# Optimization experiments

Hardware: AMD Instinct MI355X
Metric: run time of the kernel (lower is better)

## Reference

```python
import math
import jax, jax.numpy as jnp
import numpy as np

NUM_HEAD = 16
BLOCK_SIZE = 2048

def get_slopes(n):
    def pow2(n):
        start = 2 ** (-2 ** (-(math.log2(n) - 3)))
        return [start * start ** i for i in range(n)]
    if math.log2(n).is_integer():
        return pow2(n)
    c = 2 ** math.floor(math.log2(n))
    return pow2(c) + get_slopes(2 * c)[0::2][: n - c]

def setup_inputs() -> dict:
    key = jax.random.key(0)
    ks = jax.random.split(key, 5)
    B, T, C = 4, 2048, 1024
    x = jax.random.normal(ks[0], (B, T, C), dtype=jnp.float32)
    Wq = 0.02 * jax.random.normal(ks[1], (C, C), dtype=jnp.float32)
    Wk = 0.02 * jax.random.normal(ks[2], (C, C), dtype=jnp.float32)
    Wv = 0.02 * jax.random.normal(ks[3], (C, C), dtype=jnp.float32)
    Wo = 0.02 * jax.random.normal(ks[4], (C, C), dtype=jnp.float32)
    return {"x": x, "Wq": Wq, "Wk": Wk, "Wv": Wv, "Wo": Wo}

def reference(x, Wq, Wk, Wv, Wo):
    B, T, C = x.shape
    nh, hd = NUM_HEAD, C // NUM_HEAD
    # projections, split heads -> [B, nh, T, hd]
    q = (x @ Wq).reshape(B, T, nh, hd).transpose(0, 2, 1, 3)
    k = (x @ Wk).reshape(B, T, nh, hd).transpose(0, 2, 1, 3)
    v = (x @ Wv).reshape(B, T, nh, hd).transpose(0, 2, 1, 3)
    # full [B, nh, T, T] scores (module materializes these)
    attn = jnp.einsum("bhqd,bhkd->bhqk", q, k) / jnp.sqrt(jnp.float32(hd))
    # ALiBi bias as in create_mask: slope * (j - (block_size - 1)), key-position only
    slopes = jnp.asarray(get_slopes(nh), dtype=jnp.float32)  # [nh]
    bias = slopes[:, None] * (jnp.arange(T, dtype=jnp.float32) - (BLOCK_SIZE - 1))  # [nh, T]
    attn = attn + bias[None, :, None, :]
    # causal mask + stable softmax in fp32
    causal = jnp.tril(jnp.ones((T, T), dtype=bool))
    masked = jnp.where(causal[None, None], attn.astype(jnp.float32), jnp.finfo(jnp.float32).min)
    probs = jax.nn.softmax(masked, axis=-1)
    out = jnp.einsum("bhqk,bhkd->bhqd", probs, v)  # [B, nh, T, hd]
    out = out.transpose(0, 2, 1, 3).reshape(B, T, C)
    return out @ Wo
```

## Files before the change

### kernel.cpp

```cpp
#include <hip/hip_runtime.h>
#include <hip/hip_bf16.h>

#define TSEQ   2048
#define CDIM   1024
#define NHEAD  16
#define HDIM   64

typedef float f32x4  __attribute__((ext_vector_type(4)));
typedef float f32x16v __attribute__((ext_vector_type(16)));
typedef __bf16 bf16x8 __attribute__((ext_vector_type(8)));
typedef unsigned short u16x8 __attribute__((ext_vector_type(8)));
typedef unsigned short u16x4 __attribute__((ext_vector_type(4)));
typedef unsigned int   u32x4 __attribute__((ext_vector_type(4)));

#define QSCALE 0.18033688011112042f
#define LOG2E  1.4426950408889634f

static __device__ __forceinline__ unsigned short f2bf(float f) {
    unsigned u = __builtin_bit_cast(unsigned, f);
    unsigned r = u + 0x7FFFu + ((u >> 16) & 1u);
    return (unsigned short)(r >> 16);
}

static __device__ __forceinline__ f32x4 mfma16(u16x8 a, u16x8 b, f32x4 c) {
    return __builtin_amdgcn_mfma_f32_16x16x32_bf16(
        __builtin_bit_cast(bf16x8, a), __builtin_bit_cast(bf16x8, b), c, 0, 0, 0);
}
static __device__ __forceinline__ f32x16v mfma32(u16x8 a, u16x8 b, f32x16v c) {
    return __builtin_amdgcn_mfma_f32_32x32x16_bf16(
        __builtin_bit_cast(bf16x8, a), __builtin_bit_cast(bf16x8, b), c, 0, 0, 0);
}

static __device__ __forceinline__ void gload16(const void* g, void* l) {
    __builtin_amdgcn_global_load_lds(
        (const __attribute__((address_space(1))) unsigned int*)g,
        (__attribute__((address_space(3))) unsigned int*)l, 16, 0, 0);
}


__global__ __launch_bounds__(256) void castx(
    const float* __restrict__ x, unsigned short* __restrict__ xb)
{
    int t = blockIdx.x * 256 + threadIdx.x;
    f32x4 v = *(const f32x4*)&x[t * 4];
    u16x4 o;
    o[0] = f2bf(v[0]); o[1] = f2bf(v[1]); o[2] = f2bf(v[2]); o[3] = f2bf(v[3]);
    *(u16x4*)&xb[t * 4] = o;
}

__global__ __launch_bounds__(256) void wtcast(
    const float* __restrict__ wq, const float* __restrict__ wk,
    const float* __restrict__ wv, const float* __restrict__ wo,
    unsigned short* __restrict__ wt)
{
    __shared__ unsigned short t[64 * 72];
    const int z = blockIdx.z;
    const float* src = (z == 0) ? wq : (z == 1) ? wk : (z == 2) ? wv : wo;
    const int k0 = blockIdx.x * 64, n0 = blockIdx.y * 64, tid = threadIdx.x;

    #pragma unroll
    for (int i = 0; i < 4; ++i) {
        int idx = i * 256 + tid;
        int r = idx >> 4, c4 = idx & 15;
        f32x4 v = *(const f32x4*)&src[(k0 + r) * 1024 + n0 + c4 * 4];
        u16x4 o;
        o[0] = f2bf(v[0]); o[1] = f2bf(v[1]); o[2] = f2bf(v[2]); o[3] = f2bf(v[3]);
        *(u16x4*)&t[r * 72 + c4 * 4] = o;
    }
    __syncthreads();
    #pragma unroll
    for (int i = 0; i < 2; ++i) {
        int idx = i * 256 + tid;
        int n = idx >> 3, k8 = idx & 7;
        u16x8 o;
        #pragma unroll
        for (int e = 0; e < 8; ++e) o[e] = t[(k8 * 8 + e) * 72 + n];
        *(u16x8*)&wt[z * 1048576 + (n0 + n) * 1024 + k0 + k8 * 8] = o;
    }
}

template<int MODE>
__global__ __launch_bounds__(256) void gemm_gl(
    const unsigned short* __restrict__ A, const unsigned short* __restrict__ WT,
    unsigned short* __restrict__ outb, float* __restrict__ outf)
{
    __shared__ __align__(16) unsigned short Al[128 * 64];
    __shared__ __align__(16) unsigned short Bl[128 * 64];

    const int tid  = threadIdx.x;
    const int z    = blockIdx.z;
    const int m0   = blockIdx.y * 128;
    const int n0   = blockIdx.x * 128;
    const unsigned short* W = WT + (MODE == 0 ? z * 1048576 : 0);

    const int wid  = tid >> 6, lane = tid & 63;
    const int wr   = (wid >> 1) * 64, wc = (wid & 1) * 64;
    const int lrow = lane & 15, lk = (lane >> 4) * 8;

    f32x4 acc[4][4] = {};

    for (int kt = 0; kt < 16; ++kt) {
        __syncthreads();
        #pragma unroll
        for (int c = 0; c < 4; ++c) {
            int cz = wid * 4 + c;
            int row = cz * 8 + (lane >> 3), col = (lane & 7) * 8;
            gload16(&A[(m0 + row) * 1024 + kt * 64 + col], &Al[cz * 512]);
            gload16(&W[(n0 + row) * 1024 + kt * 64 + col], &Bl[cz * 512]);
        }
        __syncthreads();
        #pragma unroll
        for (int ks = 0; ks < 2; ++ks) {
            u16x8 af[4], bfr[4];
            #pragma unroll
            for (int m = 0; m < 4; ++m)
                af[m] = *(const u16x8*)&Al[(wr + m * 16 + lrow) * 64 + ks * 32 + lk];
            #pragma unroll
            for (int n = 0; n < 4; ++n)
                bfr[n] = *(const u16x8*)&Bl[(wc + n * 16 + lrow) * 64 + ks * 32 + lk];
            #pragma unroll
            for (int m = 0; m < 4; ++m)
                #pragma unroll
                for (int n = 0; n < 4; ++n)
                    acc[m][n] = mfma16(af[m], bfr[n], acc[m][n]);
        }
    }

    const int g = lane >> 4;
    #pragma unroll
    for (int m = 0; m < 4; ++m)
        #pragma unroll
        for (int n = 0; n < 4; ++n)
            #pragma unroll
            for (int j = 0; j < 4; ++j) {
                int grow = m0 + wr + m * 16 + g * 4 + j;
                int gcol = n0 + wc + n * 16 + lrow;
                float val = acc[m][n][j];
                if (MODE == 0) {
                    int b = grow >> 11, t = grow & 2047;
                    int h = gcol >> 6,  d = gcol & 63;
                    if (z == 0) val *= QSCALE;
                    if (z == 2)
                        outb[z * 8388608 + (((b << 4) + h) * 64 + d) * 2048 + t] = f2bf(val);
                    else
                        outb[z * 8388608 + (((b << 4) + h) * 2048 + t) * 64 + d] = f2bf(val);
                } else {
                    outf[grow * 1024 + gcol] = val;
                }
            }
}

__global__ __launch_bounds__(256) void attn32p(
    const unsigned short* __restrict__ qh, const unsigned short* __restrict__ kh,
    const unsigned short* __restrict__ vt, unsigned short* __restrict__ aout)
{
    __shared__ __align__(16) unsigned short Kl[2][64 * 72];
    __shared__ __align__(16) unsigned short Vl[2][64 * 72];

    const int j   = blockIdx.x;
    const int bh  = blockIdx.y;
    const int h   = bh & 15, b = bh >> 4;
    const int tid = threadIdx.x, wid = tid >> 6, lane = tid & 63;
    const int l31 = lane & 31, hi = lane >> 5;

    const int blkA = 15 - j, blkB = j;
    const int ntA  = 2 * blkA + 2;
    const int nt   = 34;

    const unsigned short* Qb = qh + bh * (TSEQ * HDIM);
    const unsigned short* Kb = kh + bh * (TSEQ * HDIM);
    const unsigned short* Vb = vt + bh * (TSEQ * HDIM);

    const float slope2 = exp2f(-0.5f * (float)(h + 1)) * LOG2E;

    int qw = blkA * 128 + wid * 32;
    int qg = qw + l31;
    u16x8 qf[4];
    #pragma unroll
    for (int kf = 0; kf < 4; ++kf)
        qf[kf] = *(const u16x8*)&Qb[qg * 64 + kf * 16 + hi * 8];
    float m_r = -1e30f, l_r = 0.f;
    f32x16v Ot[2] = {};

    #pragma unroll
    for (int i = 0; i < 2; ++i) {
        int idx = i * 256 + tid, row = idx >> 3, c8 = idx & 7;
        *(u16x8*)&Kl[0][row * 72 + c8 * 8] = *(const u16x8*)&Kb[row * 64 + c8 * 8];
        *(u16x8*)&Vl[0][row * 72 + c8 * 8] = *(const u16x8*)&Vb[row * 2048 + c8 * 8];
    }
    int cur = 0;

    for (int t = 0; t < nt; ++t) {
        const int kv0 = (t < ntA ? t : t - ntA) * 64;
        __syncthreads();

        u16x8 kreg[2], vreg[2];
        const bool pre = (t + 1 < nt);
        if (pre) {
            const int t1 = t + 1;
            const int kv0n = (t1 < ntA ? t1 : t1 - ntA) * 64;
            #pragma unroll
            for (int i = 0; i < 2; ++i) {
                int idx = i * 256 + tid, row = idx >> 3, c8 = idx & 7;
                kreg[i] = *(const u16x8*)&Kb[(kv0n + row) * 64 + c8 * 8];
                vreg[i] = *(const u16x8*)&Vb[row * 2048 + kv0n + c8 * 8];
            }
        }

        if (kv0 <= qw + 31) {
            f32x16v st[2];
            __builtin_amdgcn_s_setprio(1);
            #pragma unroll
            for (int kv2 = 0; kv2 < 2; ++kv2) {
                f32x16v a = {};
                #pragma unroll
                for (int kf = 0; kf < 4; ++kf) {
                    u16x8 ka = *(const u16x8*)&Kl[cur][(kv2 * 32 + l31) * 72 + kf * 16 + hi * 8];
                    a = mfma32(ka, qf[kf], a);
                }
                st[kv2] = a;
            }
            __builtin_amdgcn_s_setprio(0);

            const bool diag = (kv0 + 63 > qw);
            #pragma unroll
            for (int kv2 = 0; kv2 < 2; ++kv2) {
                float base = slope2 * (float)(kv0 + kv2 * 32 + 4 * hi - 2047);
                #pragma unroll
                for (int r = 0; r < 16; ++r) {
                    int koff = (r & 3) + 8 * (r >> 2);
                    float v = st[kv2][r] + fmaf(slope2, (float)koff, base);
                    if (diag) {
                        int kv = kv0 + kv2 * 32 + koff + 4 * hi;
                        if (kv > qg) v = -1e30f;
                    }
                    st[kv2][r] = v;
                }
            }

            float t8[8];
            #pragma unroll
            for (int i = 0; i < 8; ++i)
                t8[i] = fmaxf(fmaxf(st[0][i], st[0][i + 8]),
                              fmaxf(st[1][i], st[1][i + 8]));
            #pragma unroll
            for (int i = 0; i < 4; ++i) t8[i] = fmaxf(t8[i], t8[i + 4]);
            float rm = fmaxf(fmaxf(t8[0], t8[1]), fmaxf(t8[2], t8[3]));
            rm = fmaxf(rm, __shfl_xor(rm, 32, 64));

            float mn = fmaxf(m_r, rm);
            float alpha = exp2f(m_r - mn);
            m_r = mn;

            #pragma unroll
            for (int kv2 = 0; kv2 < 2; ++kv2)
                #pragma unroll
                for (int r = 0; r < 16; ++r)
                    st[kv2][r] = exp2f(st[kv2][r] - mn);
            float s8[8];
            #pragma unroll
            for (int i = 0; i < 8; ++i)
                s8[i] = (st[0][i] + st[0][i + 8]) + (st[1][i] + st[1][i + 8]);
            #pragma unroll
            for (int i = 0; i < 4; ++i) s8[i] += s8[i + 4];
            float rs = (s8[0] + s8[1]) + (s8[2] + s8[3]);
            rs += __shfl_xor(rs, 32, 64);
            l_r = l_r * alpha + rs;
            Ot[0] *= alpha;
            Ot[1] *= alpha;

            unsigned pku[2][8];
            #pragma unroll
            for (int kv2 = 0; kv2 < 2; ++kv2)
                #pragma unroll
                for (int idx = 0; idx < 8; ++idx) {
                    unsigned lo = __builtin_bit_cast(unsigned short, (__bf16)st[kv2][2 * idx]);
                    unsigned hh = __builtin_bit_cast(unsigned short, (__bf16)st[kv2][2 * idx + 1]);
                    pku[kv2][idx] = lo | (hh << 16);
                }

            u16x8 pb[4];
            #pragma unroll
            for (int kf = 0; kf < 4; ++kf) {
                const int kv2 = kf >> 1, base = 4 * (kf & 1);
                unsigned s0 = hi ? pku[kv2][base + 0] : pku[kv2][base + 2];
                unsigned s1 = hi ? pku[kv2][base + 1] : pku[kv2][base + 3];
                unsigned r0 = __shfl_xor(s0, 32, 64);
                unsigned r1 = __shfl_xor(s1, 32, 64);
                u32x4 w;
                w[0] = hi ? r0 : pku[kv2][base + 0];
                w[1] = hi ? r1 : pku[kv2][base + 1];
                w[2] = hi ? pku[kv2][base + 2] : r0;
                w[3] = hi ? pku[kv2][base + 3] : r1;
                pb[kf] = __builtin_bit_cast(u16x8, w);
            }

            __builtin_amdgcn_s_setprio(1);
            #pragma unroll
            for (int dn = 0; dn < 2; ++dn) {
                f32x16v o = Ot[dn];
                #pragma unroll
                for (int kf = 0; kf < 4; ++kf) {
                    u16x8 va = *(const u16x8*)&Vl[cur][(dn * 32 + l31) * 72 + kf * 16 + hi * 8];
                    o = mfma32(va, pb[kf], o);
                }
                Ot[dn] = o;
            }
            __builtin_amdgcn_s_setprio(0);
        }

        if (t == ntA - 1) {
            float rl = 1.0f / l_r;
            #pragma unroll
            for (int dn = 0; dn < 2; ++dn)
                #pragma unroll
                for (int rq = 0; rq < 4; ++rq) {
                    u16x4 o;
                    #pragma unroll
                    for (int jj = 0; jj < 4; ++jj)
                        o[jj] = f2bf(Ot[dn][rq * 4 + jj] * rl);
                    int d = dn * 32 + 8 * rq + 4 * hi;
                    *(u16x4*)&aout[(b * 2048 + qg) * 1024 + h * 64 + d] = o;
                }
            qw = blkB * 128 + wid * 32;
            qg = qw + l31;
            #pragma unroll
            for (int kf = 0; kf < 4; ++kf)
                qf[kf] = *(const u16x8*)&Qb[qg * 64 + kf * 16 + hi * 8];
            m_r = -1e30f; l_r = 0.f;
            Ot[0] = (f32x16v){};
            Ot[1] = (f32x16v){};
        }

        if (pre) {
            #pragma unroll
            for (int i = 0; i < 2; ++i) {
                int idx = i * 256 + tid, row = idx >> 3, c8 = idx & 7;
                *(u16x8*)&Kl[cur ^ 1][row * 72 + c8 * 8] = kreg[i];
                *(u16x8*)&Vl[cur ^ 1][row * 72 + c8 * 8] = vreg[i];
            }
        }
        cur ^= 1;
    }

    float rl = 1.0f / l_r;
    #pragma unroll
    for (int dn = 0; dn < 2; ++dn)
        #pragma unroll
        for (int rq = 0; rq < 4; ++rq) {
            u16x4 o;
            #pragma unroll
            for (int jj = 0; jj < 4; ++jj)
                o[jj] = f2bf(Ot[dn][rq * 4 + jj] * rl);
            int d = dn * 32 + 8 * rq + 4 * hi;
            *(u16x4*)&aout[(b * 2048 + qg) * 1024 + h * 64 + d] = o;
        }
}

extern "C" void kernel_launch(void* const* d_in, const int* in_sizes, int n_in,
                              void* d_out, int out_size, void* d_ws, size_t ws_size,
                              hipStream_t stream)
{
    const float* x  = (const float*)d_in[0];
    const float* Wq = (const float*)d_in[1];
    const float* Wk = (const float*)d_in[2];
    const float* Wv = (const float*)d_in[3];
    const float* Wo = (const float*)d_in[4];

    unsigned short* ws = (unsigned short*)d_ws;
    unsigned short* wb = ws;
    unsigned short* xb = ws + 4194304;
    unsigned short* qh = ws + 12582912;
    unsigned short* kh = qh + 8388608;
    unsigned short* vt = kh + 8388608;
    unsigned short* ao = xb;

    castx<<<dim3(8192), dim3(256), 0, stream>>>(x, xb);
    wtcast<<<dim3(16, 16, 4), dim3(256), 0, stream>>>(Wq, Wk, Wv, Wo, wb);
    gemm_gl<0><<<dim3(8, 64, 3), dim3(256), 0, stream>>>(xb, wb, qh, (float*)nullptr);
    attn32p<<<dim3(8, 64), dim3(256), 0, stream>>>(qh, kh, vt, ao);
    gemm_gl<1><<<dim3(8, 64, 1), dim3(256), 0, stream>>>(
        ao, wb + 3 * 1048576, (unsigned short*)nullptr, (float*)d_out);
}
```

Baseline: 248.0 us.

## Widen attention KV tiles to 128 with swizzled direct-to-LDS loads and lazy rescale

The attention kernel now processes 128-key tiles per iteration instead of 64, halving the loop trip count and the barriers per query block. K and V tiles are staged with a gload16 global-to-LDS copy into XOR-swizzled unpadded buffers instead of going through registers. The online softmax skips the max update and rescale unless the row max grows by more than 8, and the per-warp causal skip is removed, so some fully masked tiles are now computed. The cost is higher register pressure from twice as many score accumulators, plus some wasted MFMA work on masked tiles.

```diff
diff --git a/kernel.cpp b/kernel.cpp
--- a/kernel.cpp
+++ b/kernel.cpp
@@ -150,12 +150,12 @@
             }
 }
 
-__global__ __launch_bounds__(256) void attn32p(
+__global__ __launch_bounds__(256) void attn128(
     const unsigned short* __restrict__ qh, const unsigned short* __restrict__ kh,
     const unsigned short* __restrict__ vt, unsigned short* __restrict__ aout)
 {
-    __shared__ __align__(16) unsigned short Kl[2][64 * 72];
-    __shared__ __align__(16) unsigned short Vl[2][64 * 72];
+    __shared__ __align__(16) unsigned short Kl[2][128 * 64];
+    __shared__ __align__(16) unsigned short Vl[2][64 * 128];
 
     const int j   = blockIdx.x;
     const int bh  = blockIdx.y;
@@ -164,14 +164,30 @@
     const int l31 = lane & 31, hi = lane >> 5;
 
     const int blkA = 15 - j, blkB = j;
-    const int ntA  = 2 * blkA + 2;
-    const int nt   = 34;
+    const int ntA  = blkA + 1;
+    const int nt   = 17;
 
     const unsigned short* Qb = qh + bh * (TSEQ * HDIM);
     const unsigned short* Kb = kh + bh * (TSEQ * HDIM);
     const unsigned short* Vb = vt + bh * (TSEQ * HDIM);
 
     const float slope2 = exp2f(-0.5f * (float)(h + 1)) * LOG2E;
+
+    const int krow = lane >> 3;
+    const int kgc  = (lane & 7) ^ krow;
+    const int vrow = lane >> 4;
+    const int vcc  = lane & 15;
+
+#define STAGE(BUF, KV) do {                                                   \
+    _Pragma("unroll")                                                         \
+    for (int i_ = 0; i_ < 4; ++i_) {                                          \
+        int g_ = wid * 4 + i_;                                                \
+        gload16(&Kb[((KV) + g_ * 8 + krow) * 64 + kgc * 8],                   \
+                &Kl[BUF][g_ * 512]);                                          \
+        int d_ = g_ * 4 + vrow;                                               \
+        int gc_ = vcc ^ (d_ & 15);                                            \
+        gload16(&Vb[d_ * 2048 + (KV) + gc_ * 8], &Vl[BUF][g_ * 512]);         \
+    } } while (0)
 
     int qw = blkA * 128 + wid * 32;
     int qg = qw + l31;
@@ -182,132 +198,126 @@
     float m_r = -1e30f, l_r = 0.f;
     f32x16v Ot[2] = {};
 
-    #pragma unroll
-    for (int i = 0; i < 2; ++i) {
-        int idx = i * 256 + tid, row = idx >> 3, c8 = idx & 7;
-        *(u16x8*)&Kl[0][row * 72 + c8 * 8] = *(const u16x8*)&Kb[row * 64 + c8 * 8];
-        *(u16x8*)&Vl[0][row * 72 + c8 * 8] = *(const u16x8*)&Vb[row * 2048 + c8 * 8];
-    }
+    STAGE(0, 0);
     int cur = 0;
 
     for (int t = 0; t < nt; ++t) {
-        const int kv0 = (t < ntA ? t : t - ntA) * 64;
+        const int kv0 = (t < ntA ? t : t - ntA) * 128;
         __syncthreads();
 
-        u16x8 kreg[2], vreg[2];
-        const bool pre = (t + 1 < nt);
-        if (pre) {
+        if (t + 1 < nt) {
             const int t1 = t + 1;
-            const int kv0n = (t1 < ntA ? t1 : t1 - ntA) * 64;
-            #pragma unroll
-            for (int i = 0; i < 2; ++i) {
-                int idx = i * 256 + tid, row = idx >> 3, c8 = idx & 7;
-                kreg[i] = *(const u16x8*)&Kb[(kv0n + row) * 64 + c8 * 8];
-                vreg[i] = *(const u16x8*)&Vb[row * 2048 + kv0n + c8 * 8];
-            }
-        }
-
-        if (kv0 <= qw + 31) {
-            f32x16v st[2];
-            __builtin_amdgcn_s_setprio(1);
-            #pragma unroll
-            for (int kv2 = 0; kv2 < 2; ++kv2) {
-                f32x16v a = {};
-                #pragma unroll
-                for (int kf = 0; kf < 4; ++kf) {
-                    u16x8 ka = *(const u16x8*)&Kl[cur][(kv2 * 32 + l31) * 72 + kf * 16 + hi * 8];
-                    a = mfma32(ka, qf[kf], a);
+            const int kv0n = (t1 < ntA ? t1 : t1 - ntA) * 128;
+            STAGE(cur ^ 1, kv0n);
+        }
+
+        f32x16v st[4];
+        __builtin_amdgcn_s_setprio(1);
+        #pragma unroll
+        for (int kv2 = 0; kv2 < 4; ++kv2) {
+            f32x16v a = {};
+            #pragma unroll
+            for (int kf = 0; kf < 4; ++kf) {
+                u16x8 ka = *(const u16x8*)&Kl[cur][(kv2 * 32 + l31) * 64 +
+                                                   (((kf * 2 + hi) ^ (l31 & 7)) * 8)];
+                a = mfma32(ka, qf[kf], a);
+            }
+            st[kv2] = a;
+        }
+        __builtin_amdgcn_s_setprio(0);
+
+        const bool diag = (kv0 + 127 > qw);
+        #pragma unroll
+        for (int kv2 = 0; kv2 < 4; ++kv2) {
+            float base = slope2 * (float)(kv0 + kv2 * 32 + 4 * hi - 2047);
+            #pragma unroll
+            for (int r = 0; r < 16; ++r) {
+                int koff = (r & 3) + 8 * (r >> 2);
+                float v = st[kv2][r] + fmaf(slope2, (float)koff, base);
+                if (diag) {
+                    int kv = kv0 + kv2 * 32 + koff + 4 * hi;
+                    if (kv > qg) v = -1e30f;
                 }
-                st[kv2] = a;
-            }
-            __builtin_amdgcn_s_setprio(0);
-
-            const bool diag = (kv0 + 63 > qw);
-            #pragma unroll
-            for (int kv2 = 0; kv2 < 2; ++kv2) {
-                float base = slope2 * (float)(kv0 + kv2 * 32 + 4 * hi - 2047);
-                #pragma unroll
-                for (int r = 0; r < 16; ++r) {
-                    int koff = (r & 3) + 8 * (r >> 2);
-                    float v = st[kv2][r] + fmaf(slope2, (float)koff, base);
-                    if (diag) {
-                        int kv = kv0 + kv2 * 32 + koff + 4 * hi;
-                        if (kv > qg) v = -1e30f;
-                    }
-                    st[kv2][r] = v;
-                }
-            }
-
-            float t8[8];
-            #pragma unroll
-            for (int i = 0; i < 8; ++i)
-                t8[i] = fmaxf(fmaxf(st[0][i], st[0][i + 8]),
-                              fmaxf(st[1][i], st[1][i + 8]));
-            #pragma unroll
-            for (int i = 0; i < 4; ++i) t8[i] = fmaxf(t8[i], t8[i + 4]);
-            float rm = fmaxf(fmaxf(t8[0], t8[1]), fmaxf(t8[2], t8[3]));
-            rm = fmaxf(rm, __shfl_xor(rm, 32, 64));
-
+                st[kv2][r] = v;
+            }
+        }
+
+        float t16[16];
+        #pragma unroll
+        for (int i = 0; i < 16; ++i)
+            t16[i] = fmaxf(fmaxf(st[0][i], st[1][i]), fmaxf(st[2][i], st[3][i]));
+        #pragma unroll
+        for (int i = 0; i < 8; ++i) t16[i] = fmaxf(t16[i], t16[i + 8]);
+        #pragma unroll
+        for (int i = 0; i < 4; ++i) t16[i] = fmaxf(t16[i], t16[i + 4]);
+        float rm = fmaxf(fmaxf(t16[0], t16[1]), fmaxf(t16[2], t16[3]));
+        rm = fmaxf(rm, __shfl_xor(rm, 32, 64));
+
+        if (!__all(rm - m_r <= 8.0f)) {
             float mn = fmaxf(m_r, rm);
             float alpha = exp2f(m_r - mn);
             m_r = mn;
-
-            #pragma unroll
-            for (int kv2 = 0; kv2 < 2; ++kv2)
-                #pragma unroll
-                for (int r = 0; r < 16; ++r)
-                    st[kv2][r] = exp2f(st[kv2][r] - mn);
-            float s8[8];
-            #pragma unroll
-            for (int i = 0; i < 8; ++i)
-                s8[i] = (st[0][i] + st[0][i + 8]) + (st[1][i] + st[1][i + 8]);
-            #pragma unroll
-            for (int i = 0; i < 4; ++i) s8[i] += s8[i + 4];
-            float rs = (s8[0] + s8[1]) + (s8[2] + s8[3]);
-            rs += __shfl_xor(rs, 32, 64);
-            l_r = l_r * alpha + rs;
+            l_r *= alpha;
             Ot[0] *= alpha;
             Ot[1] *= alpha;
-
-            unsigned pku[2][8];
-            #pragma unroll
-            for (int kv2 = 0; kv2 < 2; ++kv2)
-                #pragma unroll
-                for (int idx = 0; idx < 8; ++idx) {
-                    unsigned lo = __builtin_bit_cast(unsigned short, (__bf16)st[kv2][2 * idx]);
-                    unsigned hh = __builtin_bit_cast(unsigned short, (__bf16)st[kv2][2 * idx + 1]);
-                    pku[kv2][idx] = lo | (hh << 16);
-                }
-
-            u16x8 pb[4];
-            #pragma unroll
-            for (int kf = 0; kf < 4; ++kf) {
-                const int kv2 = kf >> 1, base = 4 * (kf & 1);
-                unsigned s0 = hi ? pku[kv2][base + 0] : pku[kv2][base + 2];
-                unsigned s1 = hi ? pku[kv2][base + 1] : pku[kv2][base + 3];
-                unsigned r0 = __shfl_xor(s0, 32, 64);
-                unsigned r1 = __shfl_xor(s1, 32, 64);
-                u32x4 w;
-                w[0] = hi ? r0 : pku[kv2][base + 0];
-                w[1] = hi ? r1 : pku[kv2][base + 1];
-                w[2] = hi ? pku[kv2][base + 2] : r0;
-                w[3] = hi ? pku[kv2][base + 3] : r1;
-                pb[kf] = __builtin_bit_cast(u16x8, w);
-            }
-
-            __builtin_amdgcn_s_setprio(1);
-            #pragma unroll
-            for (int dn = 0; dn < 2; ++dn) {
-                f32x16v o = Ot[dn];
-                #pragma unroll
-                for (int kf = 0; kf < 4; ++kf) {
-                    u16x8 va = *(const u16x8*)&Vl[cur][(dn * 32 + l31) * 72 + kf * 16 + hi * 8];
-                    o = mfma32(va, pb[kf], o);
-                }
-                Ot[dn] = o;
-            }
-            __builtin_amdgcn_s_setprio(0);
-        }
+        }
+
+        #pragma unroll
+        for (int kv2 = 0; kv2 < 4; ++kv2)
+            #pragma unroll
+            for (int r = 0; r < 16; ++r)
+                st[kv2][r] = exp2f(st[kv2][r] - m_r);
+        float s16[16];
+        #pragma unroll
+        for (int i = 0; i < 16; ++i)
+            s16[i] = (st[0][i] + st[1][i]) + (st[2][i] + st[3][i]);
+        #pragma unroll
+        for (int i = 0; i < 8; ++i) s16[i] += s16[i + 8];
+        #pragma unroll
+        for (int i = 0; i < 4; ++i) s16[i] += s16[i + 4];
+        float rs = (s16[0] + s16[1]) + (s16[2] + s16[3]);
+        rs += __shfl_xor(rs, 32, 64);
+        l_r += rs;
+
+        unsigned pku[4][8];
+        #pragma unroll
+        for (int kv2 = 0; kv2 < 4; ++kv2)
+            #pragma unroll
+            for (int idx = 0; idx < 8; ++idx) {
+                unsigned lo = __builtin_bit_cast(unsigned short, (__bf16)st[kv2][2 * idx]);
+                unsigned hh = __builtin_bit_cast(unsigned short, (__bf16)st[kv2][2 * idx + 1]);
+                pku[kv2][idx] = lo | (hh << 16);
+            }
+
+        u16x8 pb[8];
+        #pragma unroll
+        for (int kf = 0; kf < 8; ++kf) {
+            const int kv2 = kf >> 1, base = 4 * (kf & 1);
+            unsigned s0 = hi ? pku[kv2][base + 0] : pku[kv2][base + 2];
+            unsigned s1 = hi ? pku[kv2][base + 1] : pku[kv2][base + 3];
+            unsigned r0 = __shfl_xor(s0, 32, 64);
+            unsigned r1 = __shfl_xor(s1, 32, 64);
+            u32x4 w;
+            w[0] = hi ? r0 : pku[kv2][base + 0];
+            w[1] = hi ? r1 : pku[kv2][base + 1];
+            w[2] = hi ? pku[kv2][base + 2] : r0;
+            w[3] = hi ? pku[kv2][base + 3] : r1;
+            pb[kf] = __builtin_bit_cast(u16x8, w);
+        }
+
+        __builtin_amdgcn_s_setprio(1);
+        #pragma unroll
+        for (int dn = 0; dn < 2; ++dn) {
+            f32x16v o = Ot[dn];
+            #pragma unroll
+            for (int kf = 0; kf < 8; ++kf) {
+                u16x8 va = *(const u16x8*)&Vl[cur][(dn * 32 + l31) * 128 +
+                                                   (((kf * 2 + hi) ^ (l31 & 15)) * 8)];
+                o = mfma32(va, pb[kf], o);
+            }
+            Ot[dn] = o;
+        }
+        __builtin_amdgcn_s_setprio(0);
 
         if (t == ntA - 1) {
             float rl = 1.0f / l_r;
@@ -332,14 +342,6 @@
             Ot[1] = (f32x16v){};
         }
 
-        if (pre) {
-            #pragma unroll
-            for (int i = 0; i < 2; ++i) {
-                int idx = i * 256 + tid, row = idx >> 3, c8 = idx & 7;
-                *(u16x8*)&Kl[cur ^ 1][row * 72 + c8 * 8] = kreg[i];
-                *(u16x8*)&Vl[cur ^ 1][row * 72 + c8 * 8] = vreg[i];
-            }
-        }
         cur ^= 1;
     }
 
@@ -355,6 +357,7 @@
             int d = dn * 32 + 8 * rq + 4 * hi;
             *(u16x4*)&aout[(b * 2048 + qg) * 1024 + h * 64 + d] = o;
         }
+#undef STAGE
 }
 
 extern "C" void kernel_launch(void* const* d_in, const int* in_sizes, int n_in,
@@ -378,7 +381,7 @@
     castx<<<dim3(8192), dim3(256), 0, stream>>>(x, xb);
     wtcast<<<dim3(16, 16, 4), dim3(256), 0, stream>>>(Wq, Wk, Wv, Wo, wb);
     gemm_gl<0><<<dim3(8, 64, 3), dim3(256), 0, stream>>>(xb, wb, qh, (float*)nullptr);
-    attn32p<<<dim3(8, 64), dim3(256), 0, stream>>>(qh, kh, vt, ao);
+    attn128<<<dim3(8, 64), dim3(256), 0, stream>>>(qh, kh, vt, ao);
     gemm_gl<1><<<dim3(8, 64, 1), dim3(256), 0, stream>>>(
         ao, wb + 3 * 1048576, (unsigned short*)nullptr, (float*)d_out);
 }
```

After: 238.6 us. -3.8%, faster.
